# Performance work log

Measured on AMD Instinct MI355X. Metric: run time of the kernel, lower is better.

Reference implementation:

```python
import jax, jax.numpy as jnp
import numpy as np

EPS = 1e-12  # torch F.normalize default eps

def _l2norm(x):
    n = jnp.sqrt(jnp.sum(x * x, axis=-1, keepdims=True))
    return x / jnp.maximum(n, EPS)

def setup_inputs() -> dict:
    key = jax.random.key(0)
    k1, k2, k3 = jax.random.split(key, 3)
    N, S, D = 65536, 2048, 512
    return {
        "query": jax.random.normal(k1, (N, D), dtype=jnp.float32),
        "keys": jax.random.normal(k2, (S, D), dtype=jnp.float32),
        "values": jax.random.normal(k3, (S, D), dtype=jnp.float32),
    }

def reference(query, keys, values):
    q = _l2norm(query)            # [N, D]
    k = _l2norm(keys)             # [S, D]
    scores = jnp.einsum('nd,sd->ns', q, k)   # [N, S] cosine scores
    attn = jax.nn.softmax(scores, axis=-1)   # [N, S]
    return jnp.einsum('ns,sd->nd', attn, values)  # [N, D]
```

## Files before the change

kernel.cpp:

```cpp
#include <hip/hip_runtime.h>
#include <hip/hip_bf16.h>

typedef __attribute__((ext_vector_type(8))) short short8;
typedef __attribute__((ext_vector_type(4))) float f32x4;
typedef __attribute__((ext_vector_type(2))) unsigned int u32x2;

constexpr int D_DIM = 512;
constexpr int S_DIM = 2048;

static __device__ __forceinline__ unsigned short f2bf(float f) {
  __hip_bfloat16 h = __float2bfloat16(f);
  return *reinterpret_cast<unsigned short*>(&h);
}

#define GLP(p) ((const __attribute__((address_space(1))) unsigned int*)(p))
#define LDP(p) ((__attribute__((address_space(3))) unsigned int*)(p))

static __device__ __forceinline__ void blockbar() {
  asm volatile("" ::: "memory");
  __builtin_amdgcn_s_barrier();
  asm volatile("" ::: "memory");
}

__global__ void k_norm(const float* __restrict__ K, ushort* __restrict__ Kn) {
  const int row = blockIdx.x * 4 + (threadIdx.x >> 6);
  const int l   = threadIdx.x & 63;
  const float* src = K + (size_t)row * D_DIM + l * 8;
  float4 v0 = *(const float4*)(src);
  float4 v1 = *(const float4*)(src + 4);
  float ss = v0.x*v0.x + v0.y*v0.y + v0.z*v0.z + v0.w*v0.w
           + v1.x*v1.x + v1.y*v1.y + v1.z*v1.z + v1.w*v1.w;
  #pragma unroll
  for (int off = 1; off < 64; off <<= 1) ss += __shfl_xor(ss, off, 64);
  const float sc = 1.0f / fmaxf(sqrtf(ss), 1e-12f);
  float f[8] = {v0.x,v0.y,v0.z,v0.w,v1.x,v1.y,v1.z,v1.w};
  unsigned uu[4];
  #pragma unroll
  for (int i = 0; i < 4; ++i)
    uu[i] = (unsigned)f2bf(f[2*i]*sc) | ((unsigned)f2bf(f[2*i+1]*sc) << 16);
  *(uint4*)(Kn + (size_t)row * D_DIM + l*8) = make_uint4(uu[0],uu[1],uu[2],uu[3]);
}

__global__ void k_transpose_v(const float* __restrict__ V, ushort* __restrict__ Vt) {
  __shared__ float tile[64][65];
  const int s0 = blockIdx.x * 64;
  const int d0 = blockIdx.y * 64;
  const int tj = threadIdx.x & 63;
  const int ti = threadIdx.x >> 6;
  #pragma unroll
  for (int k = 0; k < 16; ++k) {
    int s = ti + 4*k;
    tile[s][tj] = V[(size_t)(s0+s) * D_DIM + d0 + tj];
  }
  __syncthreads();
  #pragma unroll
  for (int k = 0; k < 16; ++k) {
    int d = ti + 4*k;
    Vt[(size_t)(d0+d) * S_DIM + s0 + tj] = f2bf(tile[tj][d]);
  }
}

__global__ __launch_bounds__(512, 2) void gemm1_bt(
    const ushort* __restrict__ A, const ushort* __restrict__ B,
    int aStride, int bStride,
    int NT,
    ushort* __restrict__ Pout, float* __restrict__ rowsum,
    int ldC)
{
  __shared__ ushort lds[2][4][8192];
  char* ldsb = (char*)&lds[0][0][0];

  const int tid = threadIdx.x;
  const int w   = tid >> 6;
  const int l   = tid & 63;
  const int lhi = l >> 4;
  const int llo = l & 15;
  const int wm  = w >> 2;
  const int wn  = w & 3;
  const size_t m0 = (size_t)blockIdx.x * 256;
  const size_t n0 = (size_t)blockIdx.y * 256;

  const char* Ab = (const char*)A;
  const char* Bb = (const char*)B;

  const int srow = tid >> 3;
  const int scb  = (tid & 7) * 16;
  const char* gp[4][2];
  #pragma unroll
  for (int slot = 0; slot < 4; ++slot) {
    const char* src; int stride; size_t r0;
    if (slot < 2) { src = Ab; stride = aStride; r0 = m0 + (size_t)slot * 128; }
    else          { src = Bb; stride = bStride; r0 = n0 + (size_t)(slot - 2) * 128; }
    const unsigned sw = (unsigned)(scb ^ ((srow & 7) << 4));
    gp[slot][0] = src + (r0 + srow) * (size_t)stride + sw;
    gp[slot][1] = src + (r0 + srow + 64) * (size_t)stride + sw;
  }
  auto stage = [&](int buf, int slot, int t) {
    char* lbase = ldsb + ((buf*4 + slot) * 16384) + w * 1024;
    const int toff = t * 128;
    __builtin_amdgcn_global_load_lds(GLP(gp[slot][0] + toff), LDP(lbase), 16, 0, 0);
    __builtin_amdgcn_global_load_lds(GLP(gp[slot][1] + toff), LDP(lbase + 8192), 16, 0, 0);
  };

  const unsigned swz = (unsigned)((l & 7) << 4);
  short8 ar[4][2], br01[2][2], br23[2][2];
  f32x4 acc[8][4] = {};

  const char* aBase0 = ldsb + wm * 16384;
  const char* bBase0 = ldsb + (2 + (wn >> 1)) * 16384;
  const unsigned bRow0 = (unsigned)((wn & 1) * 64);

  auto readA = [&](int buf, int rfB) {
    const char* base = aBase0 + buf * 65536;
    #pragma unroll
    for (int rf = 0; rf < 4; ++rf)
      #pragma unroll
      for (int kk = 0; kk < 2; ++kk) {
        unsigned off = (unsigned)(((rfB + rf) * 16 + llo) * 128)
                     + (((unsigned)(kk*64 + lhi*16)) ^ swz);
        ar[rf][kk] = *(const short8*)(base + off);
      }
  };
  auto readB = [&](int buf, int cfB, short8 (&br)[2][2]) {
    const char* base = bBase0 + buf * 65536;
    #pragma unroll
    for (int c = 0; c < 2; ++c)
      #pragma unroll
      for (int kk = 0; kk < 2; ++kk) {
        unsigned off = (unsigned)((bRow0 + (cfB + c) * 16 + llo) * 128)
                     + (((unsigned)(kk*64 + lhi*16)) ^ swz);
        br[c][kk] = *(const short8*)(base + off);
      }
  };
  auto quad = [&](int rfB, int cfB, short8 (&br)[2][2]) {
    __builtin_amdgcn_s_setprio(1);
    #pragma unroll
    for (int kk = 0; kk < 2; ++kk)
      #pragma unroll
      for (int rf = 0; rf < 4; ++rf)
        #pragma unroll
        for (int c = 0; c < 2; ++c)
          acc[rfB+rf][cfB+c] = __builtin_amdgcn_mfma_f32_16x16x32_bf16(
              ar[rf][kk], br[c][kk], acc[rfB+rf][cfB+c], 0, 0, 0);
    __builtin_amdgcn_s_setprio(0);
  };

  stage(0, 2, 0); stage(0, 0, 0); stage(0, 1, 0); stage(0, 3, 0);
  stage(1, 2, 1); stage(1, 0, 1);

  for (int t = 0; t < NT; ++t) {
    const int cur = t & 1, nxt = cur ^ 1;
    if (t + 1 < NT) asm volatile("s_waitcnt vmcnt(4)" ::: "memory");
    else            asm volatile("s_waitcnt vmcnt(0)" ::: "memory");
    blockbar();
    readA(cur, 0);
    readB(cur, 0, br01);
    if (t + 1 < NT) stage(nxt, 1, t + 1);
    quad(0, 0, br01);
    blockbar();
    readB(cur, 2, br23);
    if (t + 1 < NT) stage(nxt, 3, t + 1);
    quad(0, 2, br23);
    blockbar();
    readA(cur, 4);
    if (t + 2 < NT) stage(cur, 2, t + 2);
    quad(4, 2, br23);
    blockbar();
    if (t + 2 < NT) stage(cur, 0, t + 2);
    quad(4, 0, br01);
  }

  #pragma unroll
  for (int rf = 0; rf < 8; ++rf) {
    float e[4][4];
    #pragma unroll
    for (int cf = 0; cf < 4; ++cf)
      #pragma unroll
      for (int j = 0; j < 4; ++j)
        e[cf][j] = __expf(acc[rf][cf][j]);
    #pragma unroll
    for (int j = 0; j < 4; ++j) {
      const size_t m = m0 + wm*128 + rf*16 + lhi*4 + j;
      #pragma unroll
      for (int cf = 0; cf < 4; ++cf) {
        const size_t n = n0 + wn*64 + cf*16 + llo;
        Pout[m * (size_t)ldC + n] = f2bf(e[cf][j]);
      }
      float rp = (e[0][j] + e[1][j]) + (e[2][j] + e[3][j]);
      rp += __shfl_xor(rp, 1, 64);
      rp += __shfl_xor(rp, 2, 64);
      rp += __shfl_xor(rp, 4, 64);
      rp += __shfl_xor(rp, 8, 64);
      if (llo == 0) atomicAdd(&rowsum[m], rp);
    }
  }
}

__global__ __launch_bounds__(512, 2) void gemm2_bt(
    const ushort* __restrict__ A, const ushort* __restrict__ B,
    int aStride, int bStride,
    int NT,
    float* __restrict__ Oout, const float* __restrict__ rowsum,
    int ldC)
{
  __shared__ ushort lds[3][3][8192];
  char* ldsb = (char*)&lds[0][0][0];

  const int tid = threadIdx.x;
  const int w   = tid >> 6;
  const int l   = tid & 63;
  const int lhi = l >> 4;
  const int llo = l & 15;
  const int wm  = w >> 2;
  const int wn  = w & 3;
  const size_t m0 = (size_t)blockIdx.x * 128;
  const size_t n0 = (size_t)blockIdx.y * 256;

  const char* Ab = (const char*)A;
  const char* Bb = (const char*)B;

  const int srow = tid >> 3;
  const int scb  = (tid & 7) * 16;
  const char* gp[3][2];
  #pragma unroll
  for (int slot = 0; slot < 3; ++slot) {
    const char* src; int stride; size_t r0;
    if (slot == 0) { src = Ab; stride = aStride; r0 = m0; }
    else           { src = Bb; stride = bStride; r0 = n0 + (size_t)(slot - 1) * 128; }
    const unsigned sw = (unsigned)(scb ^ ((srow & 7) << 4));
    gp[slot][0] = src + (r0 + srow) * (size_t)stride + sw;
    gp[slot][1] = src + (r0 + srow + 64) * (size_t)stride + sw;
  }
  auto stage = [&](int buf, int slot, int t) {
    char* lbase = ldsb + ((buf*3 + slot) * 16384) + w * 1024;
    const int toff = t * 128;
    __builtin_amdgcn_global_load_lds(GLP(gp[slot][0] + toff), LDP(lbase), 16, 0, 0);
    __builtin_amdgcn_global_load_lds(GLP(gp[slot][1] + toff), LDP(lbase + 8192), 16, 0, 0);
  };

  const unsigned swz = (unsigned)((l & 7) << 4);
  short8 ar[4][2], br01[2][2], br23[2][2];
  f32x4 acc[4][4] = {};

  const unsigned aRow0 = (unsigned)(wm * 64);
  const int bSlot = 1 + (wn >> 1);
  const unsigned bRow0 = (unsigned)((wn & 1) * 64);

  auto readA = [&](int buf) {
    const char* base = ldsb + (buf*3) * 16384;
    #pragma unroll
    for (int rf = 0; rf < 4; ++rf)
      #pragma unroll
      for (int kk = 0; kk < 2; ++kk) {
        unsigned off = (unsigned)((aRow0 + rf*16 + llo) * 128)
                     + (((unsigned)(kk*64 + lhi*16)) ^ swz);
        ar[rf][kk] = *(const short8*)(base + off);
      }
  };
  auto readB = [&](int buf, int cfB, short8 (&br)[2][2]) {
    const char* base = ldsb + (buf*3 + bSlot) * 16384;
    #pragma unroll
    for (int c = 0; c < 2; ++c)
      #pragma unroll
      for (int kk = 0; kk < 2; ++kk) {
        unsigned off = (unsigned)((bRow0 + (cfB + c) * 16 + llo) * 128)
                     + (((unsigned)(kk*64 + lhi*16)) ^ swz);
        br[c][kk] = *(const short8*)(base + off);
      }
  };
  auto quad = [&](int cfB, short8 (&br)[2][2]) {
    __builtin_amdgcn_s_setprio(1);
    #pragma unroll
    for (int kk = 0; kk < 2; ++kk)
      #pragma unroll
      for (int rf = 0; rf < 4; ++rf)
        #pragma unroll
        for (int c = 0; c < 2; ++c)
          acc[rf][cfB+c] = __builtin_amdgcn_mfma_f32_16x16x32_bf16(
              ar[rf][kk], br[c][kk], acc[rf][cfB+c], 0, 0, 0);
    __builtin_amdgcn_s_setprio(0);
  };

  stage(0, 0, 0); stage(0, 1, 0); stage(0, 2, 0);
  stage(1, 0, 1); stage(1, 1, 1); stage(1, 2, 1);

  for (int t = 0; t < NT; ++t) {
    const int cur = t % 3, nx2 = (t + 2) % 3;
    if (t + 1 < NT) asm volatile("s_waitcnt vmcnt(6)" ::: "memory");
    else            asm volatile("s_waitcnt vmcnt(0)" ::: "memory");
    blockbar();
    readA(cur);
    readB(cur, 0, br01);
    if (t + 2 < NT) { stage(nx2, 0, t + 2); stage(nx2, 1, t + 2); }
    quad(0, br01);
    blockbar();
    readB(cur, 2, br23);
    if (t + 2 < NT) stage(nx2, 2, t + 2);
    quad(2, br23);
  }

  #pragma unroll
  for (int rf = 0; rf < 4; ++rf)
    #pragma unroll
    for (int j = 0; j < 4; ++j) {
      const size_t m = m0 + wm*64 + rf*16 + lhi*4 + j;
      const float inv = 1.0f / rowsum[m];
      #pragma unroll
      for (int cf = 0; cf < 4; ++cf) {
        const size_t n = n0 + wn*64 + cf*16 + llo;
        Oout[m * (size_t)ldC + n] = acc[rf][cf][j] * inv;
      }
    }
}

constexpr int BMf = 64, BHf = 256, NHf = S_DIM / BHf, NWf = 8;
constexpr int PBUFf = BMf * BHf * 2;

__global__ __launch_bounds__(512, 2) void attn_fused(
    const float* __restrict__ Q, const ushort* __restrict__ Kn,
    const ushort* __restrict__ Vt, float* __restrict__ out)
{
  __shared__ ushort q_s[BMf * D_DIM];
  __shared__ ushort p_s[2 * BMf * BHf];
  __shared__ float  rs_lds[NWf * BMf];
  __shared__ float  rs_tot[BMf];
  char* qb = (char*)q_s;
  char* pb = (char*)p_s;
  const int tid = threadIdx.x;
  const int w   = tid >> 6;
  const int l   = tid & 63;
  const int lhi = l >> 4;
  const int llo = l & 15;
  const size_t q0 = (size_t)blockIdx.x * BMf;
  {
    const int row = tid >> 3;
    const int c   = tid & 7;
    const unsigned swzr = (unsigned)((row & 7) << 4);
    const float4* src = (const float4*)(Q + (q0 + row) * D_DIM);
    float4 t[16];
    float ss = 0.f;
    #pragma unroll
    for (int i = 0; i < 16; ++i) {
      t[i] = src[c + i*8];
      ss += t[i].x*t[i].x + t[i].y*t[i].y + t[i].z*t[i].z + t[i].w*t[i].w;
    }
    ss += __shfl_xor(ss, 1, 64);
    ss += __shfl_xor(ss, 2, 64);
    ss += __shfl_xor(ss, 4, 64);
    const float sc = 1.0f / fmaxf(sqrtf(ss), 1e-12f);
    #pragma unroll
    for (int i = 0; i < 16; ++i) {
      u32x2 pv;
      pv[0] = (unsigned)f2bf(t[i].x*sc) | ((unsigned)f2bf(t[i].y*sc) << 16);
      pv[1] = (unsigned)f2bf(t[i].z*sc) | ((unsigned)f2bf(t[i].w*sc) << 16);
      unsigned byte = (unsigned)(row*1024) + (((unsigned)(c*8 + i*64)) ^ swzr);
      *(u32x2*)(qb + byte) = pv;
    }
  }
  __syncthreads();
  f32x4 o[4][4] = {};
  float rs_acc[4] = {0.f, 0.f, 0.f, 0.f};
  const unsigned swz = (unsigned)((l & 7) << 4);
  unsigned rowbQ[4], rowbP[4];
  #pragma unroll
  for (int qf = 0; qf < 4; ++qf) {
    rowbQ[qf] = (unsigned)((qf*16 + llo) * 1024);
    rowbP[qf] = (unsigned)((qf*16 + llo) * 512);
  }
  auto do_qkt = [&](int h, f32x4 (&sacc)[2][4]) {
    const short8* kp[2];
    #pragma unroll
    for (int kf = 0; kf < 2; ++kf)
      kp[kf] = (const short8*)(Kn + (size_t)(h*BHf + w*32 + kf*16 + llo) * D_DIM + lhi*8);
    __builtin_amdgcn_s_setprio(1);
    #pragma unroll
    for (int ks = 0; ks < 16; ++ks) {
      const unsigned off = ((unsigned)(ks*64 + lhi*16)) ^ swz;
      short8 a[2], b[4];
      #pragma unroll
      for (int kf = 0; kf < 2; ++kf) a[kf] = kp[kf][ks*4];
      #pragma unroll
      for (int qf = 0; qf < 4; ++qf)
        b[qf] = *(const short8*)(qb + (rowbQ[qf] + off));
      #pragma unroll
      for (int kf = 0; kf < 2; ++kf)
        #pragma unroll
        for (int qf = 0; qf < 4; ++qf)
          sacc[kf][qf] = __builtin_amdgcn_mfma_f32_16x16x32_bf16(a[kf], b[qf], sacc[kf][qf], 0, 0, 0);
    }
    __builtin_amdgcn_s_setprio(0);
  };
  auto do_exp = [&](f32x4 (&sacc)[2][4], u32x2 (&pk)[2][4]) {
    #pragma unroll
    for (int kf = 0; kf < 2; ++kf)
      #pragma unroll
      for (int qf = 0; qf < 4; ++qf) {
        float p0 = __expf(sacc[kf][qf][0]);
        float p1 = __expf(sacc[kf][qf][1]);
        float p2 = __expf(sacc[kf][qf][2]);
        float p3 = __expf(sacc[kf][qf][3]);
        rs_acc[qf] += (p0 + p1) + (p2 + p3);
        pk[kf][qf][0] = (unsigned)f2bf(p0) | ((unsigned)f2bf(p1) << 16);
        pk[kf][qf][1] = (unsigned)f2bf(p2) | ((unsigned)f2bf(p3) << 16);
      }
  };
  auto do_pwrite = [&](u32x2 (&pk)[2][4], char* buf) {
    #pragma unroll
    for (int kf = 0; kf < 2; ++kf)
      #pragma unroll
      for (int qf = 0; qf < 4; ++qf) {
        unsigned lin = (unsigned)(w*64 + kf*32 + lhi*8);
        *(u32x2*)(buf + rowbP[qf] + (lin ^ swz)) = pk[kf][qf];
      }
  };
  auto do_pv = [&](int h, const char* buf) {
    const short8* vp[4];
    #pragma unroll
    for (int df = 0; df < 4; ++df)
      vp[df] = (const short8*)(Vt + (size_t)(w*64 + df*16 + llo) * S_DIM + h*BHf + lhi*8);
    __builtin_amdgcn_s_setprio(1);
    #pragma unroll
    for (int ks = 0; ks < 8; ++ks) {
      const unsigned off = ((unsigned)(ks*64 + lhi*16)) ^ swz;
      short8 a[4], b[4];
      #pragma unroll
      for (int qf = 0; qf < 4; ++qf)
        a[qf] = *(const short8*)(buf + (rowbP[qf] + off));
      #pragma unroll
      for (int df = 0; df < 4; ++df) b[df] = vp[df][ks*4];
      #pragma unroll
      for (int qf = 0; qf < 4; ++qf)
        #pragma unroll
        for (int df = 0; df < 4; ++df)
          o[qf][df] = __builtin_amdgcn_mfma_f32_16x16x32_bf16(a[qf], b[df], o[qf][df], 0, 0, 0);
    }
    __builtin_amdgcn_s_setprio(0);
  };
  {
    f32x4 sacc[2][4] = {};
    do_qkt(0, sacc);
    u32x2 pk[2][4];
    do_exp(sacc, pk);
    do_pwrite(pk, pb + 0);
  }
  __syncthreads();
  for (int i = 0; i < NHf - 1; ++i) {
    f32x4 sacc[2][4] = {};
    do_qkt(i + 1, sacc);
    u32x2 pk[2][4];
    do_exp(sacc, pk);
    do_pv(i, pb + (i & 1) * PBUFf);
    do_pwrite(pk, pb + ((i + 1) & 1) * PBUFf);
    __syncthreads();
  }
  do_pv(NHf - 1, pb + ((NHf - 1) & 1) * PBUFf);
  #pragma unroll
  for (int qf = 0; qf < 4; ++qf) {
    float v = rs_acc[qf];
    v += __shfl_xor(v, 16, 64);
    v += __shfl_xor(v, 32, 64);
    if (l < 16) rs_lds[w*BMf + qf*16 + llo] = v;
  }
  __syncthreads();
  if (tid < BMf) {
    float tot = 0.f;
    #pragma unroll
    for (int ww = 0; ww < NWf; ++ww) tot += rs_lds[ww*BMf + tid];
    rs_tot[tid] = tot;
  }
  __syncthreads();
  #pragma unroll
  for (int qf = 0; qf < 4; ++qf)
    #pragma unroll
    for (int r = 0; r < 4; ++r) {
      const int query = qf*16 + lhi*4 + r;
      const float inv = 1.0f / rs_tot[query];
      #pragma unroll
      for (int df = 0; df < 4; ++df) {
        const int dim = w*64 + df*16 + llo;
        out[(q0 + query) * D_DIM + dim] = o[qf][df][r] * inv;
      }
    }
}

extern "C" void kernel_launch(void* const* d_in, const int* in_sizes, int n_in,
                              void* d_out, int out_size, void* d_ws, size_t ws_size,
                              hipStream_t stream) {
  const float* Q = (const float*)d_in[0];
  const float* K = (const float*)d_in[1];
  const float* V = (const float*)d_in[2];
  float* out = (float*)d_out;
  const int N = in_sizes[0] / D_DIM;

  ushort* Kn = (ushort*)d_ws;
  ushort* Vt = Kn + (size_t)S_DIM * D_DIM;
  char*   rest = (char*)(Vt + (size_t)D_DIM * S_DIM);
  const size_t base_bytes = (size_t)S_DIM * D_DIM * 2 * 2;
  const size_t avail = ws_size > base_bytes ? ws_size - base_bytes : 0;

  const size_t perRow = (size_t)D_DIM*2 + (size_t)S_DIM*2 + 4;
  int chunk = 0;
  const int cand[4] = {32768, 16384, 8192, 4096};
  for (int i = 0; i < 4; ++i)
    if ((size_t)cand[i] * perRow <= avail && (N % cand[i]) == 0) { chunk = cand[i]; break; }

  k_norm<<<S_DIM/4, 256, 0, stream>>>(K, Kn);
  k_transpose_v<<<dim3(S_DIM/64, D_DIM/64), 256, 0, stream>>>(V, Vt);

  if (chunk == 0) {
    attn_fused<<<N/BMf, 512, 0, stream>>>(Q, Kn, Vt, out);
    return;
  }

  ushort* Qn = (ushort*)rest;
  ushort* P  = Qn + (size_t)chunk * D_DIM;
  float* rowsum = (float*)(P + (size_t)chunk * S_DIM);

  for (int c = 0; c < N; c += chunk) {
    k_norm<<<chunk/4, 256, 0, stream>>>(Q + (size_t)c * D_DIM, Qn);
    hipMemsetAsync(rowsum, 0, (size_t)chunk * 4, stream);
    gemm1_bt<<<dim3(chunk/256, S_DIM/256), 512, 0, stream>>>(
        Qn, Kn, D_DIM*2, D_DIM*2, D_DIM/64, P, rowsum, S_DIM);
    gemm2_bt<<<dim3(chunk/128, D_DIM/256), 512, 0, stream>>>(
        P, Vt, S_DIM*2, S_DIM*2, S_DIM/64,
        out + (size_t)c * D_DIM, rowsum, D_DIM);
  }
}
```

Baseline: 382.4 us.

## Shrink gemm1 tile to 128x128 with 4 waves and simple double buffering

Rewrites the first GEMM (QK^T plus exp) to use 128x128 output tiles with 256 threads instead of 256x256 with 512 threads. The interleaved four-phase schedule is replaced by a plain double-buffered loop that waits on all loads and synchronises once per K step. The goal is more blocks, less LDS per block and more occupancy for a short K=512 reduction. The cost is lower operand reuse per block, more global traffic and less overlap of loads with compute. It also adds a 65536-row chunk candidate so the whole query set can be processed in one pass when the workspace allows.

```diff
diff --git a/kernel.cpp b/kernel.cpp
--- a/kernel.cpp
+++ b/kernel.cpp
@@ -60,14 +60,14 @@
   }
 }
 
-__global__ __launch_bounds__(512, 2) void gemm1_bt(
+__global__ __launch_bounds__(256, 2) void gemm1_bt(
     const ushort* __restrict__ A, const ushort* __restrict__ B,
     int aStride, int bStride,
     int NT,
     ushort* __restrict__ Pout, float* __restrict__ rowsum,
     int ldC)
 {
-  __shared__ ushort lds[2][4][8192];
+  __shared__ ushort lds[2][2][8192];
   char* ldsb = (char*)&lds[0][0][0];
 
   const int tid = threadIdx.x;
@@ -75,103 +75,78 @@
   const int l   = tid & 63;
   const int lhi = l >> 4;
   const int llo = l & 15;
-  const int wm  = w >> 2;
-  const int wn  = w & 3;
-  const size_t m0 = (size_t)blockIdx.x * 256;
-  const size_t n0 = (size_t)blockIdx.y * 256;
-
-  const char* Ab = (const char*)A;
-  const char* Bb = (const char*)B;
-
-  const int srow = tid >> 3;
-  const int scb  = (tid & 7) * 16;
-  const char* gp[4][2];
-  #pragma unroll
-  for (int slot = 0; slot < 4; ++slot) {
-    const char* src; int stride; size_t r0;
-    if (slot < 2) { src = Ab; stride = aStride; r0 = m0 + (size_t)slot * 128; }
-    else          { src = Bb; stride = bStride; r0 = n0 + (size_t)(slot - 2) * 128; }
-    const unsigned sw = (unsigned)(scb ^ ((srow & 7) << 4));
-    gp[slot][0] = src + (r0 + srow) * (size_t)stride + sw;
-    gp[slot][1] = src + (r0 + srow + 64) * (size_t)stride + sw;
+  const int wm  = w >> 1;
+  const int wn  = w & 1;
+  const size_t m0 = (size_t)blockIdx.x * 128;
+  const size_t n0 = (size_t)blockIdx.y * 128;
+
+  const unsigned sw = (unsigned)(((l & 7) * 16) ^ ((((unsigned)l >> 3) & 7) << 4));
+  const char* gp[2][4];
+  #pragma unroll
+  for (int slot = 0; slot < 2; ++slot) {
+    const char* src = (slot == 0) ? (const char*)A : (const char*)B;
+    const int stride = (slot == 0) ? aStride : bStride;
+    const size_t r0 = (slot == 0) ? m0 : n0;
+    #pragma unroll
+    for (int j = 0; j < 4; ++j)
+      gp[slot][j] = src + (r0 + w*32 + j*8 + (l >> 3)) * (size_t)stride + sw;
   }
   auto stage = [&](int buf, int slot, int t) {
-    char* lbase = ldsb + ((buf*4 + slot) * 16384) + w * 1024;
+    char* lbase = ldsb + ((buf*2 + slot) * 16384) + w * 4096;
     const int toff = t * 128;
-    __builtin_amdgcn_global_load_lds(GLP(gp[slot][0] + toff), LDP(lbase), 16, 0, 0);
-    __builtin_amdgcn_global_load_lds(GLP(gp[slot][1] + toff), LDP(lbase + 8192), 16, 0, 0);
+    #pragma unroll
+    for (int j = 0; j < 4; ++j)
+      __builtin_amdgcn_global_load_lds(GLP(gp[slot][j] + toff), LDP(lbase + j*1024), 16, 0, 0);
   };
 
   const unsigned swz = (unsigned)((l & 7) << 4);
-  short8 ar[4][2], br01[2][2], br23[2][2];
-  f32x4 acc[8][4] = {};
-
-  const char* aBase0 = ldsb + wm * 16384;
-  const char* bBase0 = ldsb + (2 + (wn >> 1)) * 16384;
-  const unsigned bRow0 = (unsigned)((wn & 1) * 64);
-
-  auto readA = [&](int buf, int rfB) {
-    const char* base = aBase0 + buf * 65536;
+  short8 ar[4][2], br[4][2];
+  f32x4 acc[4][4] = {};
+
+  stage(0, 0, 0); stage(0, 1, 0);
+  asm volatile("s_waitcnt vmcnt(0)" ::: "memory");
+  blockbar();
+
+  int cur = 0;
+  for (int t = 0; t < NT; ++t) {
+    if (t + 1 < NT) { stage(cur ^ 1, 0, t + 1); stage(cur ^ 1, 1, t + 1); }
+    const char* aBase = ldsb + (cur*2 + 0) * 16384;
+    const char* bBase = ldsb + (cur*2 + 1) * 16384;
     #pragma unroll
     for (int rf = 0; rf < 4; ++rf)
       #pragma unroll
       for (int kk = 0; kk < 2; ++kk) {
-        unsigned off = (unsigned)(((rfB + rf) * 16 + llo) * 128)
+        unsigned off = (unsigned)((wm*64 + rf*16 + llo) * 128)
                      + (((unsigned)(kk*64 + lhi*16)) ^ swz);
-        ar[rf][kk] = *(const short8*)(base + off);
-      }
-  };
-  auto readB = [&](int buf, int cfB, short8 (&br)[2][2]) {
-    const char* base = bBase0 + buf * 65536;
-    #pragma unroll
-    for (int c = 0; c < 2; ++c)
+        ar[rf][kk] = *(const short8*)(aBase + off);
+      }
+    #pragma unroll
+    for (int cf = 0; cf < 4; ++cf)
       #pragma unroll
       for (int kk = 0; kk < 2; ++kk) {
-        unsigned off = (unsigned)((bRow0 + (cfB + c) * 16 + llo) * 128)
+        unsigned off = (unsigned)((wn*64 + cf*16 + llo) * 128)
                      + (((unsigned)(kk*64 + lhi*16)) ^ swz);
-        br[c][kk] = *(const short8*)(base + off);
-      }
-  };
-  auto quad = [&](int rfB, int cfB, short8 (&br)[2][2]) {
+        br[cf][kk] = *(const short8*)(bBase + off);
+      }
     __builtin_amdgcn_s_setprio(1);
     #pragma unroll
     for (int kk = 0; kk < 2; ++kk)
       #pragma unroll
       for (int rf = 0; rf < 4; ++rf)
         #pragma unroll
-        for (int c = 0; c < 2; ++c)
-          acc[rfB+rf][cfB+c] = __builtin_amdgcn_mfma_f32_16x16x32_bf16(
-              ar[rf][kk], br[c][kk], acc[rfB+rf][cfB+c], 0, 0, 0);
+        for (int cf = 0; cf < 4; ++cf)
+          acc[rf][cf] = __builtin_amdgcn_mfma_f32_16x16x32_bf16(
+              ar[rf][kk], br[cf][kk], acc[rf][cf], 0, 0, 0);
     __builtin_amdgcn_s_setprio(0);
-  };
-
-  stage(0, 2, 0); stage(0, 0, 0); stage(0, 1, 0); stage(0, 3, 0);
-  stage(1, 2, 1); stage(1, 0, 1);
-
-  for (int t = 0; t < NT; ++t) {
-    const int cur = t & 1, nxt = cur ^ 1;
-    if (t + 1 < NT) asm volatile("s_waitcnt vmcnt(4)" ::: "memory");
-    else            asm volatile("s_waitcnt vmcnt(0)" ::: "memory");
-    blockbar();
-    readA(cur, 0);
-    readB(cur, 0, br01);
-    if (t + 1 < NT) stage(nxt, 1, t + 1);
-    quad(0, 0, br01);
-    blockbar();
-    readB(cur, 2, br23);
-    if (t + 1 < NT) stage(nxt, 3, t + 1);
-    quad(0, 2, br23);
-    blockbar();
-    readA(cur, 4);
-    if (t + 2 < NT) stage(cur, 2, t + 2);
-    quad(4, 2, br23);
-    blockbar();
-    if (t + 2 < NT) stage(cur, 0, t + 2);
-    quad(4, 0, br01);
-  }
-
-  #pragma unroll
-  for (int rf = 0; rf < 8; ++rf) {
+    if (t + 1 < NT) {
+      asm volatile("s_waitcnt vmcnt(0)" ::: "memory");
+      blockbar();
+      cur ^= 1;
+    }
+  }
+
+  #pragma unroll
+  for (int rf = 0; rf < 4; ++rf) {
     float e[4][4];
     #pragma unroll
     for (int cf = 0; cf < 4; ++cf)
@@ -180,7 +155,7 @@
         e[cf][j] = __expf(acc[rf][cf][j]);
     #pragma unroll
     for (int j = 0; j < 4; ++j) {
-      const size_t m = m0 + wm*128 + rf*16 + lhi*4 + j;
+      const size_t m = m0 + wm*64 + rf*16 + lhi*4 + j;
       #pragma unroll
       for (int cf = 0; cf < 4; ++cf) {
         const size_t n = n0 + wn*64 + cf*16 + llo;
@@ -500,8 +475,8 @@
 
   const size_t perRow = (size_t)D_DIM*2 + (size_t)S_DIM*2 + 4;
   int chunk = 0;
-  const int cand[4] = {32768, 16384, 8192, 4096};
-  for (int i = 0; i < 4; ++i)
+  const int cand[5] = {65536, 32768, 16384, 8192, 4096};
+  for (int i = 0; i < 5; ++i)
     if ((size_t)cand[i] * perRow <= avail && (N % cand[i]) == 0) { chunk = cand[i]; break; }
 
   k_norm<<<S_DIM/4, 256, 0, stream>>>(K, Kn);
@@ -519,7 +494,7 @@
   for (int c = 0; c < N; c += chunk) {
     k_norm<<<chunk/4, 256, 0, stream>>>(Q + (size_t)c * D_DIM, Qn);
     hipMemsetAsync(rowsum, 0, (size_t)chunk * 4, stream);
-    gemm1_bt<<<dim3(chunk/256, S_DIM/256), 512, 0, stream>>>(
+    gemm1_bt<<<dim3(chunk/128, S_DIM/128), 256, 0, stream>>>(
         Qn, Kn, D_DIM*2, D_DIM*2, D_DIM/64, P, rowsum, S_DIM);
     gemm2_bt<<<dim3(chunk/128, D_DIM/256), 512, 0, stream>>>(
         P, Vt, S_DIM*2, S_DIM*2, S_DIM/64,
```

Result: slower. 485.0 us (+26.8%).

## Make gemm1 blocks loop over multiple S tiles and enlarge gemm2 tiles

Applied to the files above, without the earlier changes.

gemm1 now launches only two column blocks, and each block sweeps four 256-wide S tiles while streaming K continuously, emitting exp/rowsum after each tile. This reduces block count and lets the A tile stay hot in cache across passes. gemm2 is switched to a 256x256 tile with double-buffered 4-slot staging, replacing the 128-row, triple-buffered version. The trade-off is fewer blocks, so per-chunk occupancy drops, and the epilogue now sits inside the main loop, which can stall the pipeline.

```diff
diff --git a/kernel.cpp b/kernel.cpp
--- a/kernel.cpp
+++ b/kernel.cpp
@@ -7,6 +7,8 @@
 
 constexpr int D_DIM = 512;
 constexpr int S_DIM = 2048;
+constexpr int NTK   = D_DIM / 64;
+constexpr int NPASS = S_DIM / (2 * 256);
 
 static __device__ __forceinline__ unsigned short f2bf(float f) {
   __hip_bfloat16 h = __float2bfloat16(f);
@@ -63,8 +65,148 @@
 __global__ __launch_bounds__(512, 2) void gemm1_bt(
     const ushort* __restrict__ A, const ushort* __restrict__ B,
     int aStride, int bStride,
+    ushort* __restrict__ Pout, float* __restrict__ rowsum,
+    int ldC)
+{
+  __shared__ ushort lds[2][4][8192];
+  char* ldsb = (char*)&lds[0][0][0];
+
+  const int tid = threadIdx.x;
+  const int w   = tid >> 6;
+  const int l   = tid & 63;
+  const int lhi = l >> 4;
+  const int llo = l & 15;
+  const int wm  = w >> 2;
+  const int wn  = w & 3;
+  const size_t m0    = (size_t)blockIdx.x * 256;
+  const size_t nbase = (size_t)blockIdx.y * (NPASS * 256);
+  constexpr int NT_TOT = NTK * NPASS;
+
+  const int srow = tid >> 3;
+  const int scb  = (tid & 7) * 16;
+  const unsigned sw = (unsigned)(scb ^ ((srow & 7) << 4));
+  const char* gp[4][2];
+  #pragma unroll
+  for (int slot = 0; slot < 4; ++slot) {
+    const char* src; int stride; size_t r0;
+    if (slot < 2) { src = (const char*)A; stride = aStride; r0 = m0 + (size_t)slot * 128; }
+    else          { src = (const char*)B; stride = bStride; r0 = nbase + (size_t)(slot - 2) * 128; }
+    gp[slot][0] = src + (r0 + srow) * (size_t)stride + sw;
+    gp[slot][1] = src + (r0 + srow + 64) * (size_t)stride + sw;
+  }
+  auto stage = [&](int buf, int slot, int t) {
+    char* lbase = ldsb + ((buf*4 + slot) * 16384) + w * 1024;
+    size_t toff;
+    if (slot < 2) toff = (size_t)(t & 7) * 128;
+    else          toff = (size_t)(t >> 3) * 256 * (size_t)bStride + (size_t)(t & 7) * 128;
+    __builtin_amdgcn_global_load_lds(GLP(gp[slot][0] + toff), LDP(lbase), 16, 0, 0);
+    __builtin_amdgcn_global_load_lds(GLP(gp[slot][1] + toff), LDP(lbase + 8192), 16, 0, 0);
+  };
+
+  const unsigned swz = (unsigned)((l & 7) << 4);
+  short8 ar[4][2], br01[2][2], br23[2][2];
+  f32x4 acc[8][4] = {};
+
+  const char* aBase0 = ldsb + wm * 16384;
+  const char* bBase0 = ldsb + (2 + (wn >> 1)) * 16384;
+  const unsigned bRow0 = (unsigned)((wn & 1) * 64);
+
+  auto readA = [&](int buf, int rfB) {
+    const char* base = aBase0 + buf * 65536;
+    #pragma unroll
+    for (int rf = 0; rf < 4; ++rf)
+      #pragma unroll
+      for (int kk = 0; kk < 2; ++kk) {
+        unsigned off = (unsigned)(((rfB + rf) * 16 + llo) * 128)
+                     + (((unsigned)(kk*64 + lhi*16)) ^ swz);
+        ar[rf][kk] = *(const short8*)(base + off);
+      }
+  };
+  auto readB = [&](int buf, int cfB, short8 (&br)[2][2]) {
+    const char* base = bBase0 + buf * 65536;
+    #pragma unroll
+    for (int c = 0; c < 2; ++c)
+      #pragma unroll
+      for (int kk = 0; kk < 2; ++kk) {
+        unsigned off = (unsigned)((bRow0 + (cfB + c) * 16 + llo) * 128)
+                     + (((unsigned)(kk*64 + lhi*16)) ^ swz);
+        br[c][kk] = *(const short8*)(base + off);
+      }
+  };
+  auto quad = [&](int rfB, int cfB, short8 (&br)[2][2]) {
+    __builtin_amdgcn_s_setprio(1);
+    #pragma unroll
+    for (int kk = 0; kk < 2; ++kk)
+      #pragma unroll
+      for (int rf = 0; rf < 4; ++rf)
+        #pragma unroll
+        for (int c = 0; c < 2; ++c)
+          acc[rfB+rf][cfB+c] = __builtin_amdgcn_mfma_f32_16x16x32_bf16(
+              ar[rf][kk], br[c][kk], acc[rfB+rf][cfB+c], 0, 0, 0);
+    __builtin_amdgcn_s_setprio(0);
+  };
+
+  stage(0, 2, 0); stage(0, 0, 0); stage(0, 1, 0); stage(0, 3, 0);
+  stage(1, 2, 1); stage(1, 0, 1);
+
+  for (int t = 0; t < NT_TOT; ++t) {
+    const int cur = t & 1, nxt = cur ^ 1;
+    if (t + 1 < NT_TOT) asm volatile("s_waitcnt vmcnt(4)" ::: "memory");
+    else                asm volatile("s_waitcnt vmcnt(0)" ::: "memory");
+    blockbar();
+    readA(cur, 0);
+    readB(cur, 0, br01);
+    if (t + 1 < NT_TOT) stage(nxt, 1, t + 1);
+    quad(0, 0, br01);
+    blockbar();
+    readB(cur, 2, br23);
+    if (t + 1 < NT_TOT) stage(nxt, 3, t + 1);
+    quad(0, 2, br23);
+    blockbar();
+    readA(cur, 4);
+    if (t + 2 < NT_TOT) stage(cur, 2, t + 2);
+    quad(4, 2, br23);
+    blockbar();
+    if (t + 2 < NT_TOT) stage(cur, 0, t + 2);
+    quad(4, 0, br01);
+
+    if ((t & (NTK - 1)) == NTK - 1) {
+      const size_t n0p = nbase + (size_t)(t >> 3) * 256;
+      #pragma unroll
+      for (int rf = 0; rf < 8; ++rf) {
+        float e[4][4];
+        #pragma unroll
+        for (int cf = 0; cf < 4; ++cf)
+          #pragma unroll
+          for (int j = 0; j < 4; ++j)
+            e[cf][j] = __expf(acc[rf][cf][j]);
+        #pragma unroll
+        for (int j = 0; j < 4; ++j) {
+          const size_t m = m0 + wm*128 + rf*16 + lhi*4 + j;
+          #pragma unroll
+          for (int cf = 0; cf < 4; ++cf) {
+            const size_t n = n0p + wn*64 + cf*16 + llo;
+            Pout[m * (size_t)ldC + n] = f2bf(e[cf][j]);
+          }
+          float rp = (e[0][j] + e[1][j]) + (e[2][j] + e[3][j]);
+          rp += __shfl_xor(rp, 1, 64);
+          rp += __shfl_xor(rp, 2, 64);
+          rp += __shfl_xor(rp, 4, 64);
+          rp += __shfl_xor(rp, 8, 64);
+          if (llo == 0) atomicAdd(&rowsum[m], rp);
+        }
+        #pragma unroll
+        for (int cf = 0; cf < 4; ++cf) acc[rf][cf] = f32x4{0.f, 0.f, 0.f, 0.f};
+      }
+    }
+  }
+}
+
+__global__ __launch_bounds__(512, 2) void gemm2_bt(
+    const ushort* __restrict__ A, const ushort* __restrict__ B,
+    int aStride, int bStride,
     int NT,
-    ushort* __restrict__ Pout, float* __restrict__ rowsum,
+    float* __restrict__ Oout, const float* __restrict__ rowsum,
     int ldC)
 {
   __shared__ ushort lds[2][4][8192];
@@ -80,24 +222,21 @@
   const size_t m0 = (size_t)blockIdx.x * 256;
   const size_t n0 = (size_t)blockIdx.y * 256;
 
-  const char* Ab = (const char*)A;
-  const char* Bb = (const char*)B;
-
   const int srow = tid >> 3;
   const int scb  = (tid & 7) * 16;
+  const unsigned sw = (unsigned)(scb ^ ((srow & 7) << 4));
   const char* gp[4][2];
   #pragma unroll
   for (int slot = 0; slot < 4; ++slot) {
     const char* src; int stride; size_t r0;
-    if (slot < 2) { src = Ab; stride = aStride; r0 = m0 + (size_t)slot * 128; }
-    else          { src = Bb; stride = bStride; r0 = n0 + (size_t)(slot - 2) * 128; }
-    const unsigned sw = (unsigned)(scb ^ ((srow & 7) << 4));
+    if (slot < 2) { src = (const char*)A; stride = aStride; r0 = m0 + (size_t)slot * 128; }
+    else          { src = (const char*)B; stride = bStride; r0 = n0 + (size_t)(slot - 2) * 128; }
     gp[slot][0] = src + (r0 + srow) * (size_t)stride + sw;
     gp[slot][1] = src + (r0 + srow + 64) * (size_t)stride + sw;
   }
   auto stage = [&](int buf, int slot, int t) {
     char* lbase = ldsb + ((buf*4 + slot) * 16384) + w * 1024;
-    const int toff = t * 128;
+    const size_t toff = (size_t)t * 128;
     __builtin_amdgcn_global_load_lds(GLP(gp[slot][0] + toff), LDP(lbase), 16, 0, 0);
     __builtin_amdgcn_global_load_lds(GLP(gp[slot][1] + toff), LDP(lbase + 8192), 16, 0, 0);
   };
@@ -171,139 +310,10 @@
   }
 
   #pragma unroll
-  for (int rf = 0; rf < 8; ++rf) {
-    float e[4][4];
-    #pragma unroll
-    for (int cf = 0; cf < 4; ++cf)
-      #pragma unroll
-      for (int j = 0; j < 4; ++j)
-        e[cf][j] = __expf(acc[rf][cf][j]);
+  for (int rf = 0; rf < 8; ++rf)
     #pragma unroll
     for (int j = 0; j < 4; ++j) {
       const size_t m = m0 + wm*128 + rf*16 + lhi*4 + j;
-      #pragma unroll
-      for (int cf = 0; cf < 4; ++cf) {
-        const size_t n = n0 + wn*64 + cf*16 + llo;
-        Pout[m * (size_t)ldC + n] = f2bf(e[cf][j]);
-      }
-      float rp = (e[0][j] + e[1][j]) + (e[2][j] + e[3][j]);
-      rp += __shfl_xor(rp, 1, 64);
-      rp += __shfl_xor(rp, 2, 64);
-      rp += __shfl_xor(rp, 4, 64);
-      rp += __shfl_xor(rp, 8, 64);
-      if (llo == 0) atomicAdd(&rowsum[m], rp);
-    }
-  }
-}
-
-__global__ __launch_bounds__(512, 2) void gemm2_bt(
-    const ushort* __restrict__ A, const ushort* __restrict__ B,
-    int aStride, int bStride,
-    int NT,
-    float* __restrict__ Oout, const float* __restrict__ rowsum,
-    int ldC)
-{
-  __shared__ ushort lds[3][3][8192];
-  char* ldsb = (char*)&lds[0][0][0];
-
-  const int tid = threadIdx.x;
-  const int w   = tid >> 6;
-  const int l   = tid & 63;
-  const int lhi = l >> 4;
-  const int llo = l & 15;
-  const int wm  = w >> 2;
-  const int wn  = w & 3;
-  const size_t m0 = (size_t)blockIdx.x * 128;
-  const size_t n0 = (size_t)blockIdx.y * 256;
-
-  const char* Ab = (const char*)A;
-  const char* Bb = (const char*)B;
-
-  const int srow = tid >> 3;
-  const int scb  = (tid & 7) * 16;
-  const char* gp[3][2];
-  #pragma unroll
-  for (int slot = 0; slot < 3; ++slot) {
-    const char* src; int stride; size_t r0;
-    if (slot == 0) { src = Ab; stride = aStride; r0 = m0; }
-    else           { src = Bb; stride = bStride; r0 = n0 + (size_t)(slot - 1) * 128; }
-    const unsigned sw = (unsigned)(scb ^ ((srow & 7) << 4));
-    gp[slot][0] = src + (r0 + srow) * (size_t)stride + sw;
-    gp[slot][1] = src + (r0 + srow + 64) * (size_t)stride + sw;
-  }
-  auto stage = [&](int buf, int slot, int t) {
-    char* lbase = ldsb + ((buf*3 + slot) * 16384) + w * 1024;
-    const int toff = t * 128;
-    __builtin_amdgcn_global_load_lds(GLP(gp[slot][0] + toff), LDP(lbase), 16, 0, 0);
-    __builtin_amdgcn_global_load_lds(GLP(gp[slot][1] + toff), LDP(lbase + 8192), 16, 0, 0);
-  };
-
-  const unsigned swz = (unsigned)((l & 7) << 4);
-  short8 ar[4][2], br01[2][2], br23[2][2];
-  f32x4 acc[4][4] = {};
-
-  const unsigned aRow0 = (unsigned)(wm * 64);
-  const int bSlot = 1 + (wn >> 1);
-  const unsigned bRow0 = (unsigned)((wn & 1) * 64);
-
-  auto readA = [&](int buf) {
-    const char* base = ldsb + (buf*3) * 16384;
-    #pragma unroll
-    for (int rf = 0; rf < 4; ++rf)
-      #pragma unroll
-      for (int kk = 0; kk < 2; ++kk) {
-        unsigned off = (unsigned)((aRow0 + rf*16 + llo) * 128)
-                     + (((unsigned)(kk*64 + lhi*16)) ^ swz);
-        ar[rf][kk] = *(const short8*)(base + off);
-      }
-  };
-  auto readB = [&](int buf, int cfB, short8 (&br)[2][2]) {
-    const char* base = ldsb + (buf*3 + bSlot) * 16384;
-    #pragma unroll
-    for (int c = 0; c < 2; ++c)
-      #pragma unroll
-      for (int kk = 0; kk < 2; ++kk) {
-        unsigned off = (unsigned)((bRow0 + (cfB + c) * 16 + llo) * 128)
-                     + (((unsigned)(kk*64 + lhi*16)) ^ swz);
-        br[c][kk] = *(const short8*)(base + off);
-      }
-  };
-  auto quad = [&](int cfB, short8 (&br)[2][2]) {
-    __builtin_amdgcn_s_setprio(1);
-    #pragma unroll
-    for (int kk = 0; kk < 2; ++kk)
-      #pragma unroll
-      for (int rf = 0; rf < 4; ++rf)
-        #pragma unroll
-        for (int c = 0; c < 2; ++c)
-          acc[rf][cfB+c] = __builtin_amdgcn_mfma_f32_16x16x32_bf16(
-              ar[rf][kk], br[c][kk], acc[rf][cfB+c], 0, 0, 0);
-    __builtin_amdgcn_s_setprio(0);
-  };
-
-  stage(0, 0, 0); stage(0, 1, 0); stage(0, 2, 0);
-  stage(1, 0, 1); stage(1, 1, 1); stage(1, 2, 1);
-
-  for (int t = 0; t < NT; ++t) {
-    const int cur = t % 3, nx2 = (t + 2) % 3;
-    if (t + 1 < NT) asm volatile("s_waitcnt vmcnt(6)" ::: "memory");
-    else            asm volatile("s_waitcnt vmcnt(0)" ::: "memory");
-    blockbar();
-    readA(cur);
-    readB(cur, 0, br01);
-    if (t + 2 < NT) { stage(nx2, 0, t + 2); stage(nx2, 1, t + 2); }
-    quad(0, br01);
-    blockbar();
-    readB(cur, 2, br23);
-    if (t + 2 < NT) stage(nx2, 2, t + 2);
-    quad(2, br23);
-  }
-
-  #pragma unroll
-  for (int rf = 0; rf < 4; ++rf)
-    #pragma unroll
-    for (int j = 0; j < 4; ++j) {
-      const size_t m = m0 + wm*64 + rf*16 + lhi*4 + j;
       const float inv = 1.0f / rowsum[m];
       #pragma unroll
       for (int cf = 0; cf < 4; ++cf) {
@@ -519,9 +529,9 @@
   for (int c = 0; c < N; c += chunk) {
     k_norm<<<chunk/4, 256, 0, stream>>>(Q + (size_t)c * D_DIM, Qn);
     hipMemsetAsync(rowsum, 0, (size_t)chunk * 4, stream);
-    gemm1_bt<<<dim3(chunk/256, S_DIM/256), 512, 0, stream>>>(
-        Qn, Kn, D_DIM*2, D_DIM*2, D_DIM/64, P, rowsum, S_DIM);
-    gemm2_bt<<<dim3(chunk/128, D_DIM/256), 512, 0, stream>>>(
+    gemm1_bt<<<dim3(chunk/256, 2), 512, 0, stream>>>(
+        Qn, Kn, D_DIM*2, D_DIM*2, P, rowsum, S_DIM);
+    gemm2_bt<<<dim3(chunk/256, D_DIM/256), 512, 0, stream>>>(
         P, Vt, S_DIM*2, S_DIM*2, S_DIM/64,
         out + (size_t)c * D_DIM, rowsum, D_DIM);
   }
```

Result: slower. 394.5 us (+3.2%).
